# Kernel tuning notes

Measured on AMD Instinct MI355X. Metric: run time of the kernel, lower is better.

## Reference

```python
import jax, jax.numpy as jnp
import numpy as np

B, C, H, W = 64, 3, 64, 64
F = 96          # base_filters
K = 8           # n_mixtures
h, w = H // 2, W // 2
C0 = 2 * C      # channels of each checkerboard half
SECTIONS = [C0, C0, C0 * K, C0 * K, C0 * K]
SPLITS = [int(s) for s in np.cumsum(SECTIONS)[:-1]]
EPS = 1e-6


def conv2d(x, wgt, b):
    y = jax.lax.conv_general_dilated(x, wgt, (1, 1), 'SAME',
                                     dimension_numbers=('NCHW', 'OIHW', 'NCHW'))
    return y + b[None, :, None, None]


def layer_norm(x, g, b, eps=1e-5):
    # nn.LayerNorm(mid_shape): normalize over (C,H,W) per sample
    mu = jnp.mean(x, axis=(1, 2, 3), keepdims=True)
    var = jnp.var(x, axis=(1, 2, 3), keepdims=True)
    return (x - mu) / jnp.sqrt(var + eps) * g[None] + b[None]


def checker_split(z, odd=False):
    Bz, Cz, Hz, Wz = z.shape
    z = z.reshape(Bz, Cz, Hz // 2, 2, Wz // 2, 2)
    p00 = z[:, :, :, 0, :, 0]; p01 = z[:, :, :, 0, :, 1]
    p10 = z[:, :, :, 1, :, 0]; p11 = z[:, :, :, 1, :, 1]
    z0 = jnp.concatenate([p00, p11], axis=1)  # even checkerboard
    z1 = jnp.concatenate([p01, p10], axis=1)  # odd checkerboard
    if odd:
        z0, z1 = z1, z0
    return z0, z1


def checker_merge(z0, z1, odd=False):
    if odd:
        z0, z1 = z1, z0
    Cz = z0.shape[1] // 2
    p00, p11 = z0[:, :Cz], z0[:, Cz:]
    p01, p10 = z1[:, :Cz], z1[:, Cz:]
    Bz, _, hz, wz = p00.shape
    zi = jnp.stack([jnp.stack([p00, p01], axis=-1),
                    jnp.stack([p10, p11], axis=-1)], axis=-2)  # (B,C,h,w,2i,2j)
    z = zi.transpose(0, 1, 2, 4, 3, 5).reshape(Bz, Cz, 2 * hz, 2 * wz)
    return z


def gated_attn(x, qkv_w, qkv_b, proj_w, proj_b):
    Bx, Fx, hx, wx = x.shape
    xf = x.reshape(Bx, Fx, hx * wx).transpose(0, 2, 1)  # (B, L, F)
    qkv = xf @ qkv_w.T + qkv_b
    q, k, v = jnp.split(qkv, 3, axis=-1)
    scores = jnp.einsum('bqf,bkf->bqk', q, k) / jnp.sqrt(jnp.float32(Fx))
    attn = jax.nn.softmax(scores, axis=-1)
    o = jnp.einsum('bqk,bkf->bqf', attn, v)
    g = o @ proj_w.T + proj_b
    ga, gb = jnp.split(g, 2, axis=-1)
    out = xf + ga * jax.nn.sigmoid(gb)  # gated residual
    return out.transpose(0, 2, 1).reshape(Bx, Fx, hx, wx)


def conditioner(z1, conv1_w, conv1_b, gconv_w, gconv_b, ln1_g, ln1_b,
                qkv_w, qkv_b, proj_w, proj_b, ln2_g, ln2_b, conv2_w, conv2_b):
    x = conv2d(z1, conv1_w, conv1_b)
    g = conv2d(x, gconv_w, gconv_b)
    ga, gb = jnp.split(g, 2, axis=1)
    x = x + ga * jax.nn.sigmoid(gb)          # GatedConv2d
    x = layer_norm(x, ln1_g, ln1_b)
    x = gated_attn(x, qkv_w, qkv_b, proj_w, proj_b)
    x = layer_norm(x, ln2_g, ln2_b)
    return conv2d(x, conv2_w, conv2_b)


def _forward(z, log_df_dz, conv1_w, conv1_b, gconv_w, gconv_b, ln1_g, ln1_b,
             qkv_w, qkv_b, proj_w, proj_b, ln2_g, ln2_b, conv2_w, conv2_b,
             a_log_scale, a_bias):
    z0, z1 = checker_split(z)
    params = conditioner(z1, conv1_w, conv1_b, gconv_w, gconv_b, ln1_g, ln1_b,
                         qkv_w, qkv_b, proj_w, proj_b, ln2_g, ln2_b, conv2_w, conv2_b)
    a, b, logpi, mu, s = jnp.split(params, SPLITS, axis=1)
    a = jnp.tanh(a) * a_log_scale + a_bias
    Bz = z0.shape[0]
    logpi = jax.nn.log_softmax(logpi.reshape(Bz, K, C0, h, w), axis=1)
    mu = mu.reshape(Bz, K, C0, h, w)
    s = s.reshape(Bz, K, C0, h, w)
    # mixture-of-logistics CDF
    u = (z0[:, None] - mu) * jnp.exp(-s)
    x = jnp.sum(jnp.exp(logpi) * jax.nn.sigmoid(u), axis=1)
    log_pdf = jax.scipy.special.logsumexp(
        logpi - s + jax.nn.log_sigmoid(u) + jax.nn.log_sigmoid(-u), axis=1)
    log_df_dz = log_df_dz + jnp.sum(log_pdf.reshape(Bz, -1), axis=1)
    # logit transform
    x = jnp.clip(x, EPS, 1.0 - EPS)
    z0n = jnp.log(x) - jnp.log1p(-x)
    log_df_dz = log_df_dz + jnp.sum((-jnp.log(x) - jnp.log1p(-x)).reshape(Bz, -1), axis=1)
    # affine rescale
    z0n = z0n * jnp.exp(a) + b
    log_df_dz = log_df_dz + jnp.sum(a.reshape(Bz, -1), axis=1)
    return checker_merge(z0n, z1), log_df_dz


def setup_inputs() -> dict:
    key = jax.random.key(0)
    ks = jax.random.split(key, 10)
    sc = 0.05
    return dict(
        z=jax.random.normal(ks[0], (B, C, H, W), jnp.float32),
        log_df_dz=jnp.zeros((B,), jnp.float32),
        conv1_w=sc * jax.random.normal(ks[1], (F, C0, 3, 3), jnp.float32),
        conv1_b=jnp.zeros((F,), jnp.float32),
        gconv_w=sc * jax.random.normal(ks[2], (2 * F, F, 3, 3), jnp.float32),
        gconv_b=jnp.zeros((2 * F,), jnp.float32),
        ln1_g=jnp.ones((F, h, w), jnp.float32),
        ln1_b=jnp.zeros((F, h, w), jnp.float32),
        qkv_w=sc * jax.random.normal(ks[3], (3 * F, F), jnp.float32),
        qkv_b=jnp.zeros((3 * F,), jnp.float32),
        proj_w=sc * jax.random.normal(ks[4], (2 * F, F), jnp.float32),
        proj_b=jnp.zeros((2 * F,), jnp.float32),
        ln2_g=jnp.ones((F, h, w), jnp.float32),
        ln2_b=jnp.zeros((F, h, w), jnp.float32),
        conv2_w=sc * jax.random.normal(ks[5], (sum(SECTIONS), F, 3, 3), jnp.float32),
        conv2_b=jnp.zeros((sum(SECTIONS),), jnp.float32),
        a_log_scale=0.01 * jax.random.normal(ks[6], (1,), jnp.float32),
        a_bias=0.01 * jax.random.normal(ks[7], (1,), jnp.float32),
    )


def reference(z, log_df_dz, conv1_w, conv1_b, gconv_w, gconv_b, ln1_g, ln1_b,
              qkv_w, qkv_b, proj_w, proj_b, ln2_g, ln2_b, conv2_w, conv2_b,
              a_log_scale, a_bias):
    return _forward(z, log_df_dz, conv1_w, conv1_b, gconv_w, gconv_b, ln1_g, ln1_b,
                    qkv_w, qkv_b, proj_w, proj_b, ln2_g, ln2_b, conv2_w, conv2_b,
                    a_log_scale, a_bias)
```

## Files before the change

kernel.cpp:

```cpp
#include <hip/hip_runtime.h>
#include <cstdint>
#include <cstddef>


typedef unsigned short u16;
typedef __attribute__((ext_vector_type(8))) short short8;
typedef __attribute__((ext_vector_type(4))) float f32x4;

__device__ __forceinline__ float sigm(float x){ return 1.0f/(1.0f+__expf(-x)); }

__device__ __forceinline__ u16 f2bf(float f){
    unsigned int u = __float_as_uint(f);
    u += 0x7fffu + ((u >> 16) & 1u);
    return (u16)(u >> 16);
}
__device__ __forceinline__ float bf2f(u16 v){
    unsigned int u = ((unsigned int)v) << 16;
    return __uint_as_float(u);
}

__global__ __launch_bounds__(256) void k_prep(
    const float* __restrict__ z, const float* __restrict__ c1w, const float* __restrict__ c1b,
    const float* __restrict__ gw, const float* __restrict__ c2w,
    const float* __restrict__ qkvw, const float* __restrict__ pw,
    const float* __restrict__ ln1g, const float* __restrict__ ln1b,
    const float* __restrict__ ln2g, const float* __restrict__ ln2b,
    const float* __restrict__ logdf,
    u16* __restrict__ x1b,
    u16* __restrict__ Wg, u16* __restrict__ W2,
    u16* __restrict__ Wqkv, u16* __restrict__ Wproj,
    float* __restrict__ gt1, float* __restrict__ bt1,
    float* __restrict__ gt2, float* __restrict__ bt2,
    float* __restrict__ outlog)
{
    int blk = blockIdx.x;
    int tid = threadIdx.x;
    __shared__ float tin[6][6][34];
    __shared__ __align__(16) u16 Wc[96][72];
    __shared__ __align__(16) u16 imc[128][72];

    if (blk < 512){
        int b  = blk >> 3;
        int pg = blk & 7;
        int r0 = pg*4;
        for (int e = tid; e < 96*72; e += 256){
            int oc = e/72, k = e%72;
            Wc[oc][k] = (k < 54) ? f2bf(c1w[oc*54 + k]) : (u16)0;
        }
        for (int idx = tid; idx < 6*6*34; idx += 256){
            int c = idx/204, rem = idx%204;
            int rr = rem/34, q = rem%34;
            int ii = r0 - 1 + rr, jj = q - 1;
            float v = 0.f;
            if ((unsigned)ii < 32u && (unsigned)jj < 32u){
                if (c < 3) v = z[((b*3+c)*64 + 2*ii)*64 + (2*jj+1)];
                else       v = z[((b*3+(c-3))*64 + (2*ii+1))*64 + 2*jj];
            }
            tin[c][rr][q] = v;
        }
        __syncthreads();
        for (int e = tid; e < 128*72; e += 256){
            int px = e/72, k = e%72;
            float v = 0.f;
            if (k < 54){
                int c = k/9, rr = (k%9)/3, dcc = k%3;
                v = tin[c][(px>>5)+rr][(px&31)+dcc];
            }
            imc[px][k] = f2bf(v);
        }
        __syncthreads();

        int w = tid >> 6, lane = tid & 63;
        int cc = lane & 15, gg = lane >> 4;
        f32x4 acc[2][6];
        #pragma unroll
        for (int u=0;u<2;++u)
            #pragma unroll
            for (int t=0;t<6;++t) acc[u][t] = (f32x4){0.f,0.f,0.f,0.f};

        #pragma unroll
        for (int ks=0; ks<2; ++ks){
            short8 a0 = *reinterpret_cast<const short8*>(&imc[w*32 + cc     ][ks*32 + 8*gg]);
            short8 a1 = *reinterpret_cast<const short8*>(&imc[w*32 + 16 + cc][ks*32 + 8*gg]);
            #pragma unroll
            for (int t=0; t<6; ++t){
                short8 bb = *reinterpret_cast<const short8*>(&Wc[t*16+cc][ks*32 + 8*gg]);
                acc[0][t] = __builtin_amdgcn_mfma_f32_16x16x32_bf16(a0, bb, acc[0][t], 0,0,0);
                acc[1][t] = __builtin_amdgcn_mfma_f32_16x16x32_bf16(a1, bb, acc[1][t], 0,0,0);
            }
        }

        #pragma unroll
        for (int u=0;u<2;++u){
            int p0 = pg*128 + w*32 + u*16 + gg*4;
            #pragma unroll
            for (int t=0;t<6;++t){
                int oc = t*16+cc;
                float bv = c1b[oc];
                #pragma unroll
                for (int r=0;r<4;++r)
                    x1b[((size_t)(b*1024) + p0 + r)*96 + oc] = f2bf(acc[u][t][r] + bv);
            }
        }
    } else if (blk < 1160){
        int idx = (blk-512)*256 + tid;
        int tap = idx / (192*96);
        int rem = idx - tap*192*96;
        int ocp = rem / 96, ic = rem % 96;
        int obk = ocp/96, r = ocp%96, isB = r/48, i = r%48;
        int oc = obk*48 + i + isB*96;
        Wg[idx] = f2bf(gw[(size_t)(oc*96+ic)*9 + tap]);
    } else if (blk < 1700){
        int idx = (blk-1160)*256 + tid;
        int tap = idx / (160*96);
        int rem = idx - tap*160*96;
        int oc = rem / 96, ic = rem % 96;
        W2[idx] = (oc < 156) ? f2bf(c2w[(size_t)(oc*96+ic)*9 + tap]) : (u16)0;
    } else if (blk < 1808){
        int idx = (blk-1700)*256 + tid;
        Wqkv[idx] = f2bf(qkvw[idx]);
    } else if (blk < 1880){
        int idx = (blk-1808)*256 + tid;
        int ocp = idx / 96, ic = idx % 96;
        int obk = ocp/96, r = ocp%96, isB = r/48, i = r%48;
        int oc = obk*48 + i + isB*96;
        Wproj[idx] = f2bf(pw[(size_t)oc*96 + ic]);
    } else if (blk < 2264){
        int idx = (blk-1880)*256 + tid;
        int c = idx >> 10, p = idx & 1023;
        gt1[p*96 + c] = ln1g[idx];
    } else if (blk < 2648){
        int idx = (blk-2264)*256 + tid;
        int c = idx >> 10, p = idx & 1023;
        bt1[p*96 + c] = ln1b[idx];
    } else if (blk < 3032){
        int idx = (blk-2648)*256 + tid;
        int c = idx >> 10, p = idx & 1023;
        gt2[p*96 + c] = ln2g[idx];
    } else if (blk < 3416){
        int idx = (blk-3032)*256 + tid;
        int c = idx >> 10, p = idx & 1023;
        bt2[p*96 + c] = ln2b[idx];
    } else {
        if (tid < 64) outlog[tid] = logdf[tid];
    }
}

__global__ __launch_bounds__(256,4) void k_gconv(const u16* __restrict__ Xpb,
    const u16* __restrict__ Wt, const float* __restrict__ bias,
    u16* __restrict__ outb, float* __restrict__ partials)
{
    int blk  = blockIdx.x;
    int obk  = blk & 1;
    int pblk = (blk >> 1) & 7;
    int b    = blk >> 4;
    int tid  = threadIdx.x;
    int w = tid >> 6, lane = tid & 63;
    int cc = lane & 15, gg = lane >> 4;

    __shared__ __align__(16) u16 Ws[96][104];
    __shared__ float red[8];

    f32x4 acc[2][6];
    #pragma unroll
    for (int u=0;u<2;++u)
        #pragma unroll
        for (int t=0;t<6;++t) acc[u][t] = (f32x4){0.f,0.f,0.f,0.f};

    int base = pblk*128 + w*32;
    int ia = base >> 5;
    const u16* xb = Xpb + (size_t)b*1024*96;
    const u16* wbase = Wt + (size_t)obk*96*96;

    short8 wreg[5];
    #pragma unroll
    for (int i=0;i<5;++i){
        int c = tid + 256*i;
        if (c < 1152){
            int oc=c/12, ico=(c%12)*8;
            wreg[i] = *reinterpret_cast<const short8*>(wbase + oc*96 + ico);
        }
    }

    for (int tap=0; tap<9; ++tap){
        int dr = tap/3 - 1, dc = tap%3 - 1;
        __syncthreads();
        #pragma unroll
        for (int i=0;i<5;++i){
            int c = tid + 256*i;
            if (c < 1152){
                int oc=c/12, ico=(c%12)*8;
                *reinterpret_cast<short8*>(&Ws[oc][ico]) = wreg[i];
            }
        }
        if (tap < 8){
            const u16* wn = wbase + (size_t)(tap+1)*192*96;
            #pragma unroll
            for (int i=0;i<5;++i){
                int c = tid + 256*i;
                if (c < 1152){
                    int oc=c/12, ico=(c%12)*8;
                    wreg[i] = *reinterpret_cast<const short8*>(wn + oc*96 + ico);
                }
            }
        }
        __syncthreads();

        int ii = ia + dr;
        int jj0 = cc + dc, jj1 = cc + 16 + dc;
        bool rv = ((unsigned)ii < 32u);
        bool v0 = rv && ((unsigned)jj0 < 32u);
        bool v1 = rv && ((unsigned)jj1 < 32u);
        const u16* ar0 = xb + (ptrdiff_t)(ii*32 + jj0)*96 + 8*gg;
        const u16* ar1 = xb + (ptrdiff_t)(ii*32 + jj1)*96 + 8*gg;

        #pragma unroll
        for (int ks=0; ks<3; ++ks){
            short8 a0 = {0,0,0,0,0,0,0,0};
            short8 a1 = {0,0,0,0,0,0,0,0};
            if (v0) a0 = *reinterpret_cast<const short8*>(ar0 + ks*32);
            if (v1) a1 = *reinterpret_cast<const short8*>(ar1 + ks*32);
            #pragma unroll
            for (int t=0; t<6; ++t){
                short8 bb = *reinterpret_cast<const short8*>(&Ws[t*16+cc][ks*32+8*gg]);
                acc[0][t] = __builtin_amdgcn_mfma_f32_16x16x32_bf16(a0, bb, acc[0][t], 0,0,0);
                acc[1][t] = __builtin_amdgcn_mfma_f32_16x16x32_bf16(a1, bb, acc[1][t], 0,0,0);
            }
        }
    }

    float s = 0.f, ssq = 0.f;
    #pragma unroll
    for (int u=0;u<2;++u){
        int p0 = base + u*16 + gg*4;
        #pragma unroll
        for (int t=0;t<3;++t){
            int ocA = obk*48 + t*16+cc;
            float ba = bias[ocA], bbv = bias[ocA+96];
            #pragma unroll
            for (int r=0;r<4;++r){
                float res = bf2f(Xpb[((size_t)b*1024 + p0+r)*96 + ocA]);
                float va = acc[u][t][r]   + ba;
                float vb = acc[u][t+3][r] + bbv;
                float v = res + va*sigm(vb);
                outb[((size_t)b*1024 + p0+r)*96 + ocA] = f2bf(v);
                s += v; ssq += v*v;
            }
        }
    }
    #pragma unroll
    for (int o=32;o>0;o>>=1){ s += __shfl_down(s,o,64); ssq += __shfl_down(ssq,o,64); }
    if (lane==0){ red[w]=s; red[4+w]=ssq; }
    __syncthreads();
    if (tid==0){
        int slot = b*16 + pblk*2 + obk;
        partials[slot*2+0] = red[0]+red[1]+red[2]+red[3];
        partials[slot*2+1] = red[4]+red[5]+red[6]+red[7];
    }
}

__global__ __launch_bounds__(256) void k_lne(const u16* __restrict__ xb,
    const float* __restrict__ gt, const float* __restrict__ bt,
    const float* __restrict__ partials, u16* __restrict__ out)
{
    int b = blockIdx.x / 48, rem = blockIdx.x % 48;
    float s=0.f, ss=0.f;
    #pragma unroll
    for (int i=0;i<16;++i){ s += partials[(b*16+i)*2]; ss += partials[(b*16+i)*2+1]; }
    float mu = s/98304.f;
    float r = rsqrtf(ss/98304.f - mu*mu + 1e-5f);

    int e8 = rem*256 + threadIdx.x;
    size_t base = (size_t)b*98304 + (size_t)e8*8;
    short8 x8 = *reinterpret_cast<const short8*>(xb + base);
    const float* gp = gt + e8*8;
    const float* bp = bt + e8*8;
    short8 o8;
    #pragma unroll
    for (int i=0;i<8;++i)
        o8[i] = (short)f2bf((bf2f((u16)x8[i]) - mu)*r*gp[i] + bp[i]);
    *reinterpret_cast<short8*>(out + base) = o8;
}

__global__ __launch_bounds__(256,4) void k_conv2m(const u16* __restrict__ Xpb,
    const u16* __restrict__ Wt, const float* __restrict__ bias,
    u16* __restrict__ out)
{
    int blk  = blockIdx.x;
    int obk  = blk & 1;
    int pblk = (blk >> 1) & 7;
    int b    = blk >> 4;
    int tid  = threadIdx.x;
    int w = tid >> 6, lane = tid & 63;
    int cc = lane & 15, gg = lane >> 4;

    __shared__ __align__(16) u16 Ws[80][104];

    f32x4 acc[2][5];
    #pragma unroll
    for (int u=0;u<2;++u)
        #pragma unroll
        for (int t=0;t<5;++t) acc[u][t] = (f32x4){0.f,0.f,0.f,0.f};

    int base = pblk*128 + w*32;
    int ia = base >> 5;
    const u16* xb = Xpb + (size_t)b*1024*96;
    const u16* wbase = Wt + (size_t)obk*80*96;

    short8 wreg[4];
    #pragma unroll
    for (int i=0;i<4;++i){
        int c = tid + 256*i;
        if (c < 960){
            int oc=c/12, ico=(c%12)*8;
            wreg[i] = *reinterpret_cast<const short8*>(wbase + oc*96 + ico);
        }
    }

    for (int tap=0; tap<9; ++tap){
        int dr = tap/3 - 1, dc = tap%3 - 1;
        __syncthreads();
        #pragma unroll
        for (int i=0;i<4;++i){
            int c = tid + 256*i;
            if (c < 960){
                int oc=c/12, ico=(c%12)*8;
                *reinterpret_cast<short8*>(&Ws[oc][ico]) = wreg[i];
            }
        }
        if (tap < 8){
            const u16* wn = wbase + (size_t)(tap+1)*160*96;
            #pragma unroll
            for (int i=0;i<4;++i){
                int c = tid + 256*i;
                if (c < 960){
                    int oc=c/12, ico=(c%12)*8;
                    wreg[i] = *reinterpret_cast<const short8*>(wn + oc*96 + ico);
                }
            }
        }
        __syncthreads();

        int ii = ia + dr;
        int jj0 = cc + dc, jj1 = cc + 16 + dc;
        bool rv = ((unsigned)ii < 32u);
        bool v0 = rv && ((unsigned)jj0 < 32u);
        bool v1 = rv && ((unsigned)jj1 < 32u);
        const u16* ar0 = xb + (ptrdiff_t)(ii*32 + jj0)*96 + 8*gg;
        const u16* ar1 = xb + (ptrdiff_t)(ii*32 + jj1)*96 + 8*gg;

        #pragma unroll
        for (int ks=0; ks<3; ++ks){
            short8 a0 = {0,0,0,0,0,0,0,0};
            short8 a1 = {0,0,0,0,0,0,0,0};
            if (v0) a0 = *reinterpret_cast<const short8*>(ar0 + ks*32);
            if (v1) a1 = *reinterpret_cast<const short8*>(ar1 + ks*32);
            #pragma unroll
            for (int t=0; t<5; ++t){
                short8 bb = *reinterpret_cast<const short8*>(&Ws[t*16+cc][ks*32+8*gg]);
                acc[0][t] = __builtin_amdgcn_mfma_f32_16x16x32_bf16(a0, bb, acc[0][t], 0,0,0);
                acc[1][t] = __builtin_amdgcn_mfma_f32_16x16x32_bf16(a1, bb, acc[1][t], 0,0,0);
            }
        }
    }

    #pragma unroll
    for (int u=0;u<2;++u){
        int p0 = base + u*16 + gg*4;
        #pragma unroll
        for (int t=0;t<5;++t){
            int oc = obk*80 + t*16+cc;
            if (oc < 156){
                float bv = bias[oc];
                u16* op = out + ((size_t)b*156 + oc)*1024 + p0;
                #pragma unroll
                for (int r=0;r<4;++r) op[r] = f2bf(acc[u][t][r] + bv);
            }
        }
    }
}

__global__ __launch_bounds__(256,4) void k_qkvm(const u16* __restrict__ Xpb,
    const u16* __restrict__ Wt, const float* __restrict__ bias,
    u16* __restrict__ Qb, u16* __restrict__ Kf, u16* __restrict__ Vf)
{
    int blk  = blockIdx.x;
    int obk  = blk & 1;
    int pblk = (blk >> 1) & 7;
    int b    = blk >> 4;
    int tid  = threadIdx.x;
    int w = tid >> 6, lane = tid & 63;
    int cc = lane & 15, gg = lane >> 4;
    const float scale = 0.10206207262f;

    __shared__ __align__(16) u16 Ws[144][104];
    {
        const u16* wp = Wt + (size_t)obk*144*96;
        for (int c = tid; c < 144*12; c += 256){
            int oc = c/12, ico = (c%12)*8;
            *reinterpret_cast<short8*>(&Ws[oc][ico]) =
                *reinterpret_cast<const short8*>(wp + oc*96 + ico);
        }
    }

    f32x4 acc[2][9];
    #pragma unroll
    for (int u=0;u<2;++u)
        #pragma unroll
        for (int t=0;t<9;++t) acc[u][t] = (f32x4){0.f,0.f,0.f,0.f};

    int base = pblk*128 + w*32;
    const u16* xb = Xpb + ((size_t)b*1024 + base)*96;
    __syncthreads();

    #pragma unroll
    for (int ks=0; ks<3; ++ks){
        short8 a0 = *reinterpret_cast<const short8*>(xb + (size_t)cc*96      + ks*32 + 8*gg);
        short8 a1 = *reinterpret_cast<const short8*>(xb + (size_t)(cc+16)*96 + ks*32 + 8*gg);
        #pragma unroll
        for (int t=0; t<9; ++t){
            short8 bb = *reinterpret_cast<const short8*>(&Ws[t*16+cc][ks*32+8*gg]);
            acc[0][t] = __builtin_amdgcn_mfma_f32_16x16x32_bf16(a0, bb, acc[0][t], 0,0,0);
            acc[1][t] = __builtin_amdgcn_mfma_f32_16x16x32_bf16(a1, bb, acc[1][t], 0,0,0);
        }
    }

    #pragma unroll
    for (int u=0;u<2;++u){
        int p0 = base + u*16 + gg*4;
        #pragma unroll
        for (int t=0;t<9;++t){
            int n = obk*144 + t*16+cc;
            float bv = bias[n];
            #pragma unroll
            for (int r=0;r<4;++r){
                int p = p0 + r;
                float av = acc[u][t][r] + bv;
                if (n < 96){
                    Qb[((size_t)(b*1024+p))*96 + n] = f2bf(av*scale);
                } else if (n < 192){
                    int f = n-96;
                    int jt = p>>6, t16 = (p>>4)&3, ccs = p&15;
                    int ks = f>>5, ggs = (f>>3)&3, j = f&7;
                    Kf[(size_t)(b*16+jt)*6144 + (size_t)(((t16*3+ks)*4+ggs)*16+ccs)*8 + j] = f2bf(av);
                } else {
                    int f = n-192;
                    int jt = p>>6, kl = p&63;
                    int kk = kl>>5, ggs = (kl>>3)&3, j = kl&7;
                    int ft = f>>4, ccs = f&15;
                    Vf[(size_t)(b*16+jt)*6144 + (size_t)(((ft*2+kk)*4+ggs)*16+ccs)*8 + j] = f2bf(av);
                }
            }
        }
    }
}

__global__ __launch_bounds__(256,4) void k_attn(const u16* __restrict__ Qb,
    const u16* __restrict__ Kf, const u16* __restrict__ Vf, u16* __restrict__ Ob)
{
    int qt = blockIdx.x >> 6;
    int b  = blockIdx.x & 63;
    int tid = threadIdx.x;
    int w  = tid >> 6;
    int lane = tid & 63;
    int cc = lane & 15;
    int gg = lane >> 4;

    __shared__ __align__(16) u16 Ks[6144];
    __shared__ __align__(16) u16 Vs[6144];
    __shared__ __align__(16) u16 Ps[4][2048];

    int q0 = qt*64 + w*16;

    short8 qf[3];
    {
        const u16* qrow = Qb + ((size_t)(b*1024 + q0 + cc))*96;
        #pragma unroll
        for (int ks=0; ks<3; ++ks)
            qf[ks] = *reinterpret_cast<const short8*>(qrow + ks*32 + 8*gg);
    }

    f32x4 Oacc[6];
    #pragma unroll
    for (int ft=0; ft<6; ++ft) Oacc[ft] = (f32x4){0.f,0.f,0.f,0.f};
    float l_r[4] = {0.f,0.f,0.f,0.f};

    const u16* Kb0 = Kf + (size_t)(b*16)*6144;
    const u16* Vb0 = Vf + (size_t)(b*16)*6144;

    short8 kreg[3], vreg[3];
    #pragma unroll
    for (int i=0;i<3;++i){
        int s8 = (tid + 256*i)*8;
        kreg[i] = *reinterpret_cast<const short8*>(Kb0 + s8);
        vreg[i] = *reinterpret_cast<const short8*>(Vb0 + s8);
    }

    for (int jt=0; jt<16; ++jt){
        __syncthreads();
        #pragma unroll
        for (int i=0;i<3;++i){
            int s8 = (tid + 256*i)*8;
            *reinterpret_cast<short8*>(Ks + s8) = kreg[i];
            *reinterpret_cast<short8*>(Vs + s8) = vreg[i];
        }
        if (jt < 15){
            const u16* kn = Kb0 + (size_t)(jt+1)*6144;
            const u16* vn = Vb0 + (size_t)(jt+1)*6144;
            #pragma unroll
            for (int i=0;i<3;++i){
                int s8 = (tid + 256*i)*8;
                kreg[i] = *reinterpret_cast<const short8*>(kn + s8);
                vreg[i] = *reinterpret_cast<const short8*>(vn + s8);
            }
        }
        __syncthreads();

        f32x4 Sacc[4];
        #pragma unroll
        for (int t=0;t<4;++t) Sacc[t] = (f32x4){0.f,0.f,0.f,0.f};
        #pragma unroll
        for (int ks=0; ks<3; ++ks){
            #pragma unroll
            for (int t=0; t<4; ++t){
                short8 bb = *reinterpret_cast<const short8*>(Ks + ((t*3+ks)*64 + lane)*8);
                Sacc[t] = __builtin_amdgcn_mfma_f32_16x16x32_bf16(qf[ks], bb, Sacc[t], 0,0,0);
            }
        }

        #pragma unroll
        for (int t=0; t<4; ++t){
            int kk = t>>1;
            int ggs = ((t&1)<<1) | (cc>>3);
            int jj = cc&7;
            #pragma unroll
            for (int r=0; r<4; ++r){
                float p = __expf(Sacc[t][r]);
                l_r[r] += p;
                Ps[w][((kk*4 + ggs)*16 + (4*gg+r))*8 + jj] = f2bf(p);
            }
        }

        #pragma unroll
        for (int kk=0; kk<2; ++kk){
            short8 pa = *reinterpret_cast<const short8*>(&Ps[w][(kk*64 + lane)*8]);
            #pragma unroll
            for (int ft=0; ft<6; ++ft){
                short8 vb = *reinterpret_cast<const short8*>(Vs + ((ft*2+kk)*64 + lane)*8);
                Oacc[ft] = __builtin_amdgcn_mfma_f32_16x16x32_bf16(pa, vb, Oacc[ft], 0,0,0);
            }
        }
    }

    #pragma unroll
    for (int r=0; r<4; ++r){
        #pragma unroll
        for (int msk=1; msk<16; msk<<=1) l_r[r] += __shfl_xor(l_r[r], msk, 64);
    }
    float linv[4];
    #pragma unroll
    for (int r=0; r<4; ++r) linv[r] = 1.0f / l_r[r];
    #pragma unroll
    for (int ft=0; ft<6; ++ft)
        #pragma unroll
        for (int r=0; r<4; ++r)
            Ob[((size_t)(b*1024 + q0 + 4*gg + r))*96 + ft*16 + cc]
                = f2bf(Oacc[ft][r]*linv[r]);
}

__global__ __launch_bounds__(256,4) void k_projm(const u16* __restrict__ Opb,
    const u16* __restrict__ Wt, const float* __restrict__ bias,
    const u16* __restrict__ xlnb, u16* __restrict__ outb, float* __restrict__ partials)
{
    int blk  = blockIdx.x;
    int obk  = blk & 1;
    int pblk = (blk >> 1) & 7;
    int b    = blk >> 4;
    int tid  = threadIdx.x;
    int w = tid >> 6, lane = tid & 63;
    int cc = lane & 15, gg = lane >> 4;

    __shared__ __align__(16) u16 Ws[96][104];
    __shared__ float red[8];
    {
        const u16* wp = Wt + (size_t)obk*96*96;
        for (int c = tid; c < 96*12; c += 256){
            int oc = c/12, ico = (c%12)*8;
            *reinterpret_cast<short8*>(&Ws[oc][ico]) =
                *reinterpret_cast<const short8*>(wp + oc*96 + ico);
        }
    }

    f32x4 acc[2][6];
    #pragma unroll
    for (int u=0;u<2;++u)
        #pragma unroll
        for (int t=0;t<6;++t) acc[u][t] = (f32x4){0.f,0.f,0.f,0.f};

    int base = pblk*128 + w*32;
    const u16* xb = Opb + ((size_t)b*1024 + base)*96;
    __syncthreads();

    #pragma unroll
    for (int ks=0; ks<3; ++ks){
        short8 a0 = *reinterpret_cast<const short8*>(xb + (size_t)cc*96      + ks*32 + 8*gg);
        short8 a1 = *reinterpret_cast<const short8*>(xb + (size_t)(cc+16)*96 + ks*32 + 8*gg);
        #pragma unroll
        for (int t=0; t<6; ++t){
            short8 bb = *reinterpret_cast<const short8*>(&Ws[t*16+cc][ks*32+8*gg]);
            acc[0][t] = __builtin_amdgcn_mfma_f32_16x16x32_bf16(a0, bb, acc[0][t], 0,0,0);
            acc[1][t] = __builtin_amdgcn_mfma_f32_16x16x32_bf16(a1, bb, acc[1][t], 0,0,0);
        }
    }

    const u16* resb = xlnb + (size_t)b*1024*96;
    float s = 0.f, ssq = 0.f;
    #pragma unroll
    for (int u=0;u<2;++u){
        int p0 = base + u*16 + gg*4;
        #pragma unroll
        for (int t=0;t<3;++t){
            int ocA = obk*48 + t*16+cc;
            float ba = bias[ocA], bbv = bias[ocA+96];
            #pragma unroll
            for (int r=0;r<4;++r){
                float ga = acc[u][t][r]   + ba;
                float gb = acc[u][t+3][r] + bbv;
                float res = bf2f(resb[(size_t)(p0+r)*96 + ocA]);
                float v = res + ga * sigm(gb);
                outb[((size_t)b*1024 + p0+r)*96 + ocA] = f2bf(v);
                s += v; ssq += v*v;
            }
        }
    }
    #pragma unroll
    for (int o=32;o>0;o>>=1){ s += __shfl_down(s,o,64); ssq += __shfl_down(ssq,o,64); }
    if (lane==0){ red[w]=s; red[4+w]=ssq; }
    __syncthreads();
    if (tid==0){
        int slot = b*16 + pblk*2 + obk;
        partials[slot*2+0] = red[0]+red[1]+red[2]+red[3];
        partials[slot*2+1] = red[4]+red[5]+red[6]+red[7];
    }
}

__global__ __launch_bounds__(256) void k_mix(const float* __restrict__ z,
    const u16* __restrict__ params, const float* __restrict__ a_ls_p,
    const float* __restrict__ a_b_p, float* __restrict__ out_z, float* __restrict__ out_log)
{
    int b = blockIdx.x / 24;
    int rem = blockIdx.x % 24;
    int c0 = rem / 4;
    int pix = (rem & 3)*256 + threadIdx.x;
    int i = pix >> 5, j = pix & 31;
    float als = a_ls_p[0], abv = a_b_p[0];
    const u16* pb = params + (size_t)b*156*1024;
    float logacc = 0.f;

    if (c0 < 3){
        int idx01 = ((b*3+c0)*64 + 2*i)*64 + 2*j+1;
        int idx10 = ((b*3+c0)*64 + 2*i+1)*64 + 2*j;
        out_z[idx01] = z[idx01];
        out_z[idx10] = z[idx10];
    }

    {
        float z0v = (c0<3) ? z[((b*3+c0)*64 + 2*i)*64 + 2*j]
                           : z[((b*3+(c0-3))*64 + 2*i+1)*64 + 2*j+1];
        float a_raw = bf2f(pb[(c0)*1024 + pix]);
        float bco   = bf2f(pb[(6+c0)*1024 + pix]);
        float lp[8], mu[8], sv[8];
        float m1 = -1e30f;
        #pragma unroll
        for (int k=0;k<8;++k){
            lp[k] = bf2f(pb[(12 + k*6 + c0)*1024 + pix]);
            mu[k] = bf2f(pb[(60 + k*6 + c0)*1024 + pix]);
            sv[k] = bf2f(pb[(108 + k*6 + c0)*1024 + pix]);
            m1 = fmaxf(m1, lp[k]);
        }
        float se = 0.f;
        #pragma unroll
        for (int k=0;k<8;++k) se += __expf(lp[k]-m1);
        float lse = m1 + __logf(se);
        float xm = 0.f, mt = -1e30f;
        float t[8];
        #pragma unroll
        for (int k=0;k<8;++k){
            float lpn = lp[k] - lse;
            float u = (z0v - mu[k]) * __expf(-sv[k]);
            float au = fabsf(u);
            xm += __expf(lpn) * (1.f/(1.f+__expf(-u)));
            float lss = -(au + 2.f*log1pf(__expf(-au)));
            float tk = lpn - sv[k] + lss;
            t[k] = tk; mt = fmaxf(mt, tk);
        }
        float se2 = 0.f;
        #pragma unroll
        for (int k=0;k<8;++k) se2 += __expf(t[k]-mt);
        logacc += mt + __logf(se2);
        xm = fminf(fmaxf(xm, 1e-6f), 1.f-1e-6f);
        float lx = __logf(xm), l1x = log1pf(-xm);
        logacc += -lx - l1x;
        float aa = tanhf(a_raw)*als + abv;
        float z0n = (lx - l1x)*__expf(aa) + bco;
        logacc += aa;
        int oidx = (c0<3) ? ((b*3+c0)*64 + 2*i)*64 + 2*j
                          : ((b*3+(c0-3))*64 + 2*i+1)*64 + 2*j+1;
        out_z[oidx] = z0n;
    }

    #pragma unroll
    for (int o=32;o>0;o>>=1) logacc += __shfl_down(logacc, o, 64);
    __shared__ float part[4];
    if ((threadIdx.x&63)==0) part[threadIdx.x>>6] = logacc;
    __syncthreads();
    if (threadIdx.x==0){
        atomicAdd(out_log + b, part[0]+part[1]+part[2]+part[3]);
    }
}

extern "C" void kernel_launch(void* const* d_in, const int* in_sizes, int n_in,
                              void* d_out, int out_size, void* d_ws, size_t ws_size,
                              hipStream_t stream)
{
    const float* z     = (const float*)d_in[0];
    const float* logdf = (const float*)d_in[1];
    const float* c1w   = (const float*)d_in[2];
    const float* c1b   = (const float*)d_in[3];
    const float* gw    = (const float*)d_in[4];
    const float* gcb   = (const float*)d_in[5];
    const float* ln1g  = (const float*)d_in[6];
    const float* ln1b  = (const float*)d_in[7];
    const float* qkvw  = (const float*)d_in[8];
    const float* qkvb  = (const float*)d_in[9];
    const float* pw    = (const float*)d_in[10];
    const float* pbb   = (const float*)d_in[11];
    const float* ln2g  = (const float*)d_in[12];
    const float* ln2b  = (const float*)d_in[13];
    const float* c2w   = (const float*)d_in[14];
    const float* c2b   = (const float*)d_in[15];
    const float* als   = (const float*)d_in[16];
    const float* ab    = (const float*)d_in[17];

    float* out_z   = (float*)d_out;
    float* out_log = out_z + 786432;

    float* ws     = (float*)d_ws;
    u16*   x1b    = (u16*)(ws + 0);
    u16*   xg_b   = (u16*)(ws + 3145728);
    u16*   xlnb   = (u16*)(ws + 6291456);
    u16*   Vf     = (u16*)(ws + 9437184);
    u16*   Ob     = (u16*)(ws + 12582912);
    u16*   x2b    = (u16*)(ws + 15728640);
    u16*   Qb     = x1b;
    u16*   Kf     = xg_b;
    u16*   xln2b  = xlnb;
    u16*   params = (u16*)(ws + 9437184);
    const size_t T = 19660800;
    float* gt1    = ws + T;
    float* bt1    = ws + T + 98304;
    float* gt2    = ws + T + 196608;
    float* bt2    = ws + T + 294912;
    float* part1  = ws + T + 393216;
    float* part2  = ws + T + 395264;
    u16*   Wg     = (u16*)(ws + T + 397568);
    u16*   W2     = (u16*)(ws + T + 480512);
    u16*   Wqkv   = (u16*)(ws + T + 549632);
    u16*   Wproj  = (u16*)(ws + T + 563456);

    k_prep   <<<3417, 256, 0, stream>>>(z, c1w, c1b, gw, c2w, qkvw, pw,
                                        ln1g, ln1b, ln2g, ln2b, logdf,
                                        x1b, Wg, W2, Wqkv, Wproj,
                                        gt1, bt1, gt2, bt2, out_log);
    k_gconv  <<<1024, 256, 0, stream>>>(x1b, Wg, gcb, xg_b, part1);
    k_lne    <<<3072, 256, 0, stream>>>(xg_b, gt1, bt1, part1, xlnb);
    k_qkvm   <<<1024, 256, 0, stream>>>(xlnb, Wqkv, qkvb, Qb, Kf, Vf);
    k_attn   <<<1024, 256, 0, stream>>>(Qb, Kf, Vf, Ob);
    k_projm  <<<1024, 256, 0, stream>>>(Ob, Wproj, pbb, xlnb, x2b, part2);
    k_lne    <<<3072, 256, 0, stream>>>(x2b, gt2, bt2, part2, xln2b);
    k_conv2m <<<1024, 256, 0, stream>>>(xln2b, W2, c2b, params);
    k_mix    <<<1536, 256, 0, stream>>>(z, params, als, ab, out_z, out_log);
}
```

Measured before the change: 282.7 us.

## Switch attention kernel to 32x32x16 MFMA tiles with 128-thread blocks

The attention kernel now uses 32x32x16 bf16 MFMA instead of 16x16x32. Each wave covers 32 queries, and blocks shrink to two waves covering 64 queries. The K and V fragment layouts written by the QKV kernel are rearranged to match the new operand format, and the P staging buffer is padded. The aim is fewer MFMA issues and fewer LDS reads of K/V per unit of work, at the cost of more registers per thread and lower occupancy (launch bounds 128,2).

```diff
diff --git a/kernel.cpp b/kernel.cpp
--- a/kernel.cpp
+++ b/kernel.cpp
@@ -6,6 +6,7 @@
 typedef unsigned short u16;
 typedef __attribute__((ext_vector_type(8))) short short8;
 typedef __attribute__((ext_vector_type(4))) float f32x4;
+typedef __attribute__((ext_vector_type(16))) float f32x16;
 
 __device__ __forceinline__ float sigm(float x){ return 1.0f/(1.0f+__expf(-x)); }
 
@@ -440,22 +441,25 @@
                     Qb[((size_t)(b*1024+p))*96 + n] = f2bf(av*scale);
                 } else if (n < 192){
                     int f = n-96;
-                    int jt = p>>6, t16 = (p>>4)&3, ccs = p&15;
-                    int ks = f>>5, ggs = (f>>3)&3, j = f&7;
-                    Kf[(size_t)(b*16+jt)*6144 + (size_t)(((t16*3+ks)*4+ggs)*16+ccs)*8 + j] = f2bf(av);
+                    int jt = p>>6, kl = p&63;
+                    int tt = kl>>5;
+                    int lanep = (kl&31) + 32*((f>>3)&1);
+                    int ks = f>>4, j = f&7;
+                    Kf[(size_t)(b*16+jt)*6144 + (size_t)(((tt*6+ks)*64 + lanep))*8 + j] = f2bf(av);
                 } else {
                     int f = n-192;
                     int jt = p>>6, kl = p&63;
-                    int kk = kl>>5, ggs = (kl>>3)&3, j = kl&7;
-                    int ft = f>>4, ccs = f&15;
-                    Vf[(size_t)(b*16+jt)*6144 + (size_t)(((ft*2+kk)*4+ggs)*16+ccs)*8 + j] = f2bf(av);
+                    int ks2 = kl>>4, hi = (kl>>3)&1, j = kl&7;
+                    int ft2 = f>>5;
+                    int lanep = (f&31) + 32*hi;
+                    Vf[(size_t)(b*16+jt)*6144 + (size_t)(((ft2*4+ks2)*64 + lanep))*8 + j] = f2bf(av);
                 }
             }
         }
     }
 }
 
-__global__ __launch_bounds__(256,4) void k_attn(const u16* __restrict__ Qb,
+__global__ __launch_bounds__(128,2) void k_attn(const u16* __restrict__ Qb,
     const u16* __restrict__ Kf, const u16* __restrict__ Vf, u16* __restrict__ Ob)
 {
     int qt = blockIdx.x >> 6;
@@ -463,35 +467,39 @@
     int tid = threadIdx.x;
     int w  = tid >> 6;
     int lane = tid & 63;
-    int cc = lane & 15;
-    int gg = lane >> 4;
+    int ln32 = lane & 31;
+    int hl = lane >> 5;
 
     __shared__ __align__(16) u16 Ks[6144];
     __shared__ __align__(16) u16 Vs[6144];
-    __shared__ __align__(16) u16 Ps[4][2048];
-
-    int q0 = qt*64 + w*16;
-
-    short8 qf[3];
+    __shared__ __align__(16) u16 Ps[2][2112];
+
+    int q0 = qt*64 + w*32;
+
+    short8 qf[6];
     {
-        const u16* qrow = Qb + ((size_t)(b*1024 + q0 + cc))*96;
-        #pragma unroll
-        for (int ks=0; ks<3; ++ks)
-            qf[ks] = *reinterpret_cast<const short8*>(qrow + ks*32 + 8*gg);
-    }
-
-    f32x4 Oacc[6];
-    #pragma unroll
-    for (int ft=0; ft<6; ++ft) Oacc[ft] = (f32x4){0.f,0.f,0.f,0.f};
-    float l_r[4] = {0.f,0.f,0.f,0.f};
+        const u16* qrow = Qb + ((size_t)(b*1024 + q0 + ln32))*96 + hl*8;
+        #pragma unroll
+        for (int ks=0; ks<6; ++ks)
+            qf[ks] = *reinterpret_cast<const short8*>(qrow + ks*16);
+    }
+
+    f32x16 Oacc[3];
+    #pragma unroll
+    for (int ft=0; ft<3; ++ft)
+        #pragma unroll
+        for (int r=0; r<16; ++r) Oacc[ft][r] = 0.f;
+    float l_acc[16];
+    #pragma unroll
+    for (int r=0; r<16; ++r) l_acc[r] = 0.f;
 
     const u16* Kb0 = Kf + (size_t)(b*16)*6144;
     const u16* Vb0 = Vf + (size_t)(b*16)*6144;
 
-    short8 kreg[3], vreg[3];
-    #pragma unroll
-    for (int i=0;i<3;++i){
-        int s8 = (tid + 256*i)*8;
+    short8 kreg[6], vreg[6];
+    #pragma unroll
+    for (int i=0;i<6;++i){
+        int s8 = (tid + 128*i)*8;
         kreg[i] = *reinterpret_cast<const short8*>(Kb0 + s8);
         vreg[i] = *reinterpret_cast<const short8*>(Vb0 + s8);
     }
@@ -499,8 +507,8 @@
     for (int jt=0; jt<16; ++jt){
         __syncthreads();
         #pragma unroll
-        for (int i=0;i<3;++i){
-            int s8 = (tid + 256*i)*8;
+        for (int i=0;i<6;++i){
+            int s8 = (tid + 128*i)*8;
             *reinterpret_cast<short8*>(Ks + s8) = kreg[i];
             *reinterpret_cast<short8*>(Vs + s8) = vreg[i];
         }
@@ -508,64 +516,65 @@
             const u16* kn = Kb0 + (size_t)(jt+1)*6144;
             const u16* vn = Vb0 + (size_t)(jt+1)*6144;
             #pragma unroll
-            for (int i=0;i<3;++i){
-                int s8 = (tid + 256*i)*8;
+            for (int i=0;i<6;++i){
+                int s8 = (tid + 128*i)*8;
                 kreg[i] = *reinterpret_cast<const short8*>(kn + s8);
                 vreg[i] = *reinterpret_cast<const short8*>(vn + s8);
             }
         }
         __syncthreads();
 
-        f32x4 Sacc[4];
-        #pragma unroll
-        for (int t=0;t<4;++t) Sacc[t] = (f32x4){0.f,0.f,0.f,0.f};
-        #pragma unroll
-        for (int ks=0; ks<3; ++ks){
-            #pragma unroll
-            for (int t=0; t<4; ++t){
-                short8 bb = *reinterpret_cast<const short8*>(Ks + ((t*3+ks)*64 + lane)*8);
-                Sacc[t] = __builtin_amdgcn_mfma_f32_16x16x32_bf16(qf[ks], bb, Sacc[t], 0,0,0);
-            }
-        }
-
-        #pragma unroll
-        for (int t=0; t<4; ++t){
-            int kk = t>>1;
-            int ggs = ((t&1)<<1) | (cc>>3);
-            int jj = cc&7;
-            #pragma unroll
-            for (int r=0; r<4; ++r){
+        f32x16 Sacc[2];
+        #pragma unroll
+        for (int t=0;t<2;++t)
+            #pragma unroll
+            for (int r=0;r<16;++r) Sacc[t][r] = 0.f;
+        #pragma unroll
+        for (int ks=0; ks<6; ++ks){
+            #pragma unroll
+            for (int t=0; t<2; ++t){
+                short8 bb = *reinterpret_cast<const short8*>(Ks + ((t*6+ks)*64 + lane)*8);
+                Sacc[t] = __builtin_amdgcn_mfma_f32_32x32x16_bf16(qf[ks], bb, Sacc[t], 0,0,0);
+            }
+        }
+
+        #pragma unroll
+        for (int t=0; t<2; ++t){
+            int off0 = (t*2 + (ln32>>4))*528 + ((ln32>>3)&1)*264 + (lane&7);
+            #pragma unroll
+            for (int r=0; r<16; ++r){
+                int q = 4*hl + (r&3) + 8*(r>>2);
                 float p = __expf(Sacc[t][r]);
-                l_r[r] += p;
-                Ps[w][((kk*4 + ggs)*16 + (4*gg+r))*8 + jj] = f2bf(p);
-            }
-        }
-
-        #pragma unroll
-        for (int kk=0; kk<2; ++kk){
-            short8 pa = *reinterpret_cast<const short8*>(&Ps[w][(kk*64 + lane)*8]);
-            #pragma unroll
-            for (int ft=0; ft<6; ++ft){
-                short8 vb = *reinterpret_cast<const short8*>(Vs + ((ft*2+kk)*64 + lane)*8);
-                Oacc[ft] = __builtin_amdgcn_mfma_f32_16x16x32_bf16(pa, vb, Oacc[ft], 0,0,0);
-            }
-        }
-    }
-
-    #pragma unroll
-    for (int r=0; r<4; ++r){
-        #pragma unroll
-        for (int msk=1; msk<16; msk<<=1) l_r[r] += __shfl_xor(l_r[r], msk, 64);
-    }
-    float linv[4];
-    #pragma unroll
-    for (int r=0; r<4; ++r) linv[r] = 1.0f / l_r[r];
-    #pragma unroll
-    for (int ft=0; ft<6; ++ft)
-        #pragma unroll
-        for (int r=0; r<4; ++r)
-            Ob[((size_t)(b*1024 + q0 + 4*gg + r))*96 + ft*16 + cc]
-                = f2bf(Oacc[ft][r]*linv[r]);
+                l_acc[r] += p;
+                Ps[w][off0 + q*8] = f2bf(p);
+            }
+        }
+
+        #pragma unroll
+        for (int ks2=0; ks2<4; ++ks2){
+            short8 pa = *reinterpret_cast<const short8*>(&Ps[w][ks2*528 + hl*264 + ln32*8]);
+            #pragma unroll
+            for (int ft=0; ft<3; ++ft){
+                short8 vb = *reinterpret_cast<const short8*>(Vs + ((ft*4+ks2)*64 + lane)*8);
+                Oacc[ft] = __builtin_amdgcn_mfma_f32_32x32x16_bf16(pa, vb, Oacc[ft], 0,0,0);
+            }
+        }
+    }
+
+    #pragma unroll
+    for (int r=0; r<16; ++r){
+        #pragma unroll
+        for (int msk=1; msk<32; msk<<=1)
+            l_acc[r] += __shfl_xor(l_acc[r], msk, 64);
+    }
+    #pragma unroll
+    for (int r=0; r<16; ++r){
+        int q = 4*hl + (r&3) + 8*(r>>2);
+        float linv = 1.0f / l_acc[r];
+        #pragma unroll
+        for (int ft=0; ft<3; ++ft)
+            Ob[((size_t)(b*1024 + q0 + q))*96 + ft*32 + ln32] = f2bf(Oacc[ft][r]*linv);
+    }
 }
 
 __global__ __launch_bounds__(256,4) void k_projm(const u16* __restrict__ Opb,
@@ -775,7 +784,7 @@
     k_gconv  <<<1024, 256, 0, stream>>>(x1b, Wg, gcb, xg_b, part1);
     k_lne    <<<3072, 256, 0, stream>>>(xg_b, gt1, bt1, part1, xlnb);
     k_qkvm   <<<1024, 256, 0, stream>>>(xlnb, Wqkv, qkvb, Qb, Kf, Vf);
-    k_attn   <<<1024, 256, 0, stream>>>(Qb, Kf, Vf, Ob);
+    k_attn   <<<1024, 128, 0, stream>>>(Qb, Kf, Vf, Ob);
     k_projm  <<<1024, 256, 0, stream>>>(Ob, Wproj, pbb, xlnb, x2b, part2);
     k_lne    <<<3072, 256, 0, stream>>>(x2b, gt2, bt2, part2, xln2b);
     k_conv2m <<<1024, 256, 0, stream>>>(xln2b, W2, c2b, params);
```

Result: slower. 290.2 us (+2.6%).
